# Kernel optimization log

Hardware: AMD Instinct MI355X
Metric: run time of the kernel (lower is better)

The kernel has to match this reference:

```python
import jax, jax.numpy as jnp
import numpy as np

N, E = 20000, 320000      # nodes, edges (avg degree 16)
IN_DIM, N_HID = 256, 256
T, R, H, L = 8, 8, 8, 2   # node types, relations, heads, layers
DK = N_HID // H


def _type_linear(x, W, b, ntype):
    # x:[N,di], W:[T,di,do], b:[T,do] -> per-node-type linear (compute-all + select;
    # math identical to the original boolean-mask gather->Linear->scatter dispatch)
    y_all = jnp.einsum('nd,tdo->nto', x, W) + b[None]
    return jnp.take_along_axis(y_all, ntype[:, None, None], axis=1)[:, 0]


def _mblock(x, ntype, edge_index, etype, ew, kW, kb, qW, qb, vW, vb, aW, ab,
            rel_pri, rel_att, rel_msg, skip, ln_g, ln_b):
    n, d = x.shape
    src, dst = edge_index[0], edge_index[1]
    k = _type_linear(x, kW, kb, ntype).reshape(n, H, DK)
    q = _type_linear(x, qW, qb, ntype).reshape(n, H, DK)
    v = _type_linear(x, vW, vb, ntype).reshape(n, H, DK)
    # relation-transformed keys/messages at node level: [N,R,H,DK]
    k_rt = jnp.einsum('nhd,rhde->nrhe', k, rel_att)
    v_rt = jnp.einsum('nhd,rhde->nrhe', v, rel_msg)
    k_e = k_rt[src, etype]          # [E,H,DK]
    v_e = v_rt[src, etype]          # [E,H,DK]
    q_e = q[dst]                    # [E,H,DK]
    scores = jnp.einsum('ehd,ehd->eh', q_e, k_e) * rel_pri[etype] / np.sqrt(DK)
    scores = scores * ew[:, None]   # edge weighting of attention logits
    # segment softmax over incoming edges of each destination node
    smax = jax.ops.segment_max(scores, dst, num_segments=n)
    ex = jnp.exp(scores - smax[dst])
    ssum = jax.ops.segment_sum(ex, dst, num_segments=n)
    att = ex / (ssum[dst] + 1e-9)   # [E,H]
    agg = jax.ops.segment_sum(att[:, :, None] * v_e, dst, num_segments=n).reshape(n, d)
    trans = _type_linear(jax.nn.gelu(agg), aW, ab, ntype)
    alpha = jax.nn.sigmoid(skip)[ntype][:, None]
    out = trans * alpha + x * (1.0 - alpha)
    # per-type LayerNorm
    mu = out.mean(-1, keepdims=True)
    var = out.var(-1, keepdims=True)
    out = (out - mu) / jnp.sqrt(var + 1e-5) * ln_g[ntype] + ln_b[ntype]
    return out, att


def setup_inputs():
    key = jax.random.key(0)
    ks = jax.random.split(key, 16)
    s = 0.05
    return {
        'node_feature': jax.random.normal(ks[0], (N, IN_DIM), jnp.float32),
        'node_type':    jax.random.randint(ks[1], (N,), 0, T, jnp.int32),
        'edge_weight':  jax.random.uniform(ks[2], (E,), jnp.float32),
        'edge_index':   jax.random.randint(ks[3], (2, E), 0, N, jnp.int32),
        'edge_type':    jax.random.randint(ks[4], (E,), 0, R, jnp.int32),
        'adapt_W': jax.random.normal(ks[5], (T, IN_DIM, N_HID), jnp.float32) * s,
        'adapt_b': jnp.zeros((T, N_HID), jnp.float32),
        'k_W': jax.random.normal(ks[6], (L, T, N_HID, N_HID), jnp.float32) * s,
        'k_b': jnp.zeros((L, T, N_HID), jnp.float32),
        'q_W': jax.random.normal(ks[7], (L, T, N_HID, N_HID), jnp.float32) * s,
        'q_b': jnp.zeros((L, T, N_HID), jnp.float32),
        'v_W': jax.random.normal(ks[8], (L, T, N_HID, N_HID), jnp.float32) * s,
        'v_b': jnp.zeros((L, T, N_HID), jnp.float32),
        'a_W': jax.random.normal(ks[9], (L, T, N_HID, N_HID), jnp.float32) * s,
        'a_b': jnp.zeros((L, T, N_HID), jnp.float32),
        'rel_pri': jnp.ones((L, R, H), jnp.float32),
        'rel_att': jax.random.normal(ks[10], (L, R, H, DK, DK), jnp.float32) * 0.1,
        'rel_msg': jax.random.normal(ks[11], (L, R, H, DK, DK), jnp.float32) * 0.1,
        'skip': jnp.ones((L, T), jnp.float32),
        'ln_g': jnp.ones((L, T, N_HID), jnp.float32),
        'ln_b': jnp.zeros((L, T, N_HID), jnp.float32),
    }


def reference(node_feature, node_type, edge_weight, edge_index, edge_type,
              adapt_W, adapt_b, k_W, k_b, q_W, q_b, v_W, v_b, a_W, a_b,
              rel_pri, rel_att, rel_msg, skip, ln_g, ln_b):
    # type-dispatched adapt: gather -> Linear -> tanh -> scatter (vectorized)
    x = jnp.tanh(_type_linear(node_feature, adapt_W, adapt_b, node_type))
    att = None
    for l in range(L):  # fixed small n_layers
        x, att = _mblock(x, node_type, edge_index, edge_type, edge_weight,
                         k_W[l], k_b[l], q_W[l], q_b[l], v_W[l], v_b[l],
                         a_W[l], a_b[l], rel_pri[l], rel_att[l], rel_msg[l],
                         skip[l], ln_g[l], ln_b[l])
    return x, att
```

## Files before the change

### kernel.cpp

```cpp
#include <hip/hip_runtime.h>
#include <hip/hip_bf16.h>
#include <math.h>

#define NN 20000
#define EE 320000
#define DD 256
#define TT 8
#define RR 8
#define HH 8
#define LLAYERS 2
#define RELN (LLAYERS * RR * HH * 1024)
#define NBN 79

typedef __attribute__((ext_vector_type(8))) short short8;
typedef __attribute__((ext_vector_type(4))) float f32x4;
typedef __attribute__((ext_vector_type(4))) unsigned short us4;

__device__ __forceinline__ float b2f(unsigned short u) {
    return __uint_as_float(((unsigned int)u) << 16);
}
__device__ __forceinline__ unsigned short f2b(float f) {
    unsigned int x = __float_as_uint(f);
    unsigned int r = (x + 0x7fffu + ((x >> 16) & 1u)) >> 16;
    return (unsigned short)r;
}

__global__ void k_prep(const float* __restrict__ nf, const float* __restrict__ rA,
                       const float* __restrict__ rM,
                       unsigned short* __restrict__ nf_bf, unsigned short* __restrict__ relA,
                       unsigned short* __restrict__ relMT) {
    int idx = blockIdx.x * 256 + threadIdx.x;
    const int n0 = NN * 256;
    if (idx < n0) { nf_bf[idx] = f2b(nf[idx]); return; }
    idx -= n0;
    if (idx < RELN) { relA[idx] = f2b(rA[idx]); return; }
    idx -= RELN;
    if (idx < RELN) {
        int g = idx >> 10, loc = idx & 1023;
        int a = loc >> 5, b = loc & 31;
        relMT[(size_t)g * 1024 + a * 32 + b] = f2b(rM[(size_t)g * 1024 + b * 32 + a]);
    }
}

__global__ void k_transpose_all(const float* __restrict__ adW, const float* __restrict__ kW,
                                const float* __restrict__ qW, const float* __restrict__ vW,
                                const float* __restrict__ aW, unsigned short* __restrict__ out) {
    __shared__ float tile[32][33];
    int z = blockIdx.z;
    const float* ip;
    if (z < 8) ip = adW + (size_t)z * 65536;
    else if (z < 24) ip = kW + (size_t)(z - 8) * 65536;
    else if (z < 40) ip = qW + (size_t)(z - 24) * 65536;
    else if (z < 56) ip = vW + (size_t)(z - 40) * 65536;
    else ip = aW + (size_t)(z - 56) * 65536;
    unsigned short* op = out + (size_t)z * 65536;
    int ox = blockIdx.x * 32, dy = blockIdx.y * 32;
    int tx = threadIdx.x, ty = threadIdx.y;
#pragma unroll
    for (int r = 0; r < 4; r++) tile[ty + 8 * r][tx] = ip[(size_t)(dy + ty + 8 * r) * 256 + ox + tx];
    __syncthreads();
#pragma unroll
    for (int r = 0; r < 4; r++) op[(size_t)(ox + ty + 8 * r) * 256 + dy + tx] = f2b(tile[tx][ty + 8 * r]);
}

__global__ void k_build1(const int* __restrict__ ei, const int* __restrict__ nt,
                         int* __restrict__ deg8, int* __restrict__ thist,
                         int* __restrict__ rank) {
    __shared__ int ltc[TT];
    int i = blockIdx.x * 256 + threadIdx.x;
    int vx = blockIdx.x & 7;
    if (i < EE) {
        int d = ei[EE + i];
        int lr = atomicAdd(&deg8[vx * NN + d], 1);
        rank[i] = (vx << 16) | lr;
    }
    if (blockIdx.x < NBN) {
        if (threadIdx.x < TT) ltc[threadIdx.x] = 0;
        __syncthreads();
        int n = blockIdx.x * 256 + threadIdx.x;
        if (n < NN) atomicAdd(&ltc[nt[n]], 1);
        __syncthreads();
        if (threadIdx.x < TT) thist[blockIdx.x * TT + threadIdx.x] = ltc[threadIdx.x];
    }
}

__global__ __launch_bounds__(256) void k_scanA(const int* __restrict__ deg8,
                                               int* __restrict__ degT,
                                               int* __restrict__ bsum) {
    __shared__ int red[256];
    int b = blockIdx.x, t = threadIdx.x;
    int n = b * 256 + t;
    int tot = 0;
    if (n < NN) {
#pragma unroll
        for (int vx = 0; vx < 8; vx++) tot += deg8[vx * NN + n];
        degT[n] = tot;
    }
    red[t] = tot;
    __syncthreads();
    for (int d = 128; d >= 1; d >>= 1) {
        if (t < d) red[t] += red[t + d];
        __syncthreads();
    }
    if (t == 0) bsum[b] = red[0];
}

__global__ void k_scanB(const int* __restrict__ bsum, int* __restrict__ bbase,
                        int* __restrict__ off,
                        const int* __restrict__ thist, int* __restrict__ toff,
                        int* __restrict__ tboff) {
    __shared__ int partial[TT];
    __shared__ int toff_l[TT + 1];
    int tid = threadIdx.x;
    if (tid == 0) {
        int a = 0;
        for (int b = 0; b < NBN; b++) { bbase[b] = a; a += bsum[b]; }
        off[NN] = EE;
    }
    if (tid < TT) {
        int tot = 0;
        for (int b = 0; b < NBN; b++) tot += thist[b * TT + tid];
        partial[tid] = tot;
    }
    __syncthreads();
    if (tid == 0) {
        int a = 0;
        for (int t = 0; t < TT; t++) { toff_l[t] = a; toff[t] = a; a += partial[t]; }
        toff_l[TT] = a; toff[TT] = a;
    }
    __syncthreads();
    if (tid < TT) {
        int r = toff_l[tid];
        for (int b = 0; b < NBN; b++) { tboff[b * TT + tid] = r; r += thist[b * TT + tid]; }
    }
}

__global__ __launch_bounds__(256) void k_scanC(const int* __restrict__ deg8,
                                               const int* __restrict__ degT,
                                               const int* __restrict__ bbase,
                                               int* __restrict__ off,
                                               int* __restrict__ base8) {
    __shared__ int s[256];
    int b = blockIdx.x, t = threadIdx.x;
    int n = b * 256 + t;
    int v = (n < NN) ? degT[n] : 0;
    s[t] = v;
    __syncthreads();
    for (int d = 1; d < 256; d <<= 1) {
        int x = (t >= d) ? s[t - d] : 0;
        __syncthreads();
        s[t] += x;
        __syncthreads();
    }
    if (n < NN) {
        int run = bbase[b] + s[t] - v;
        off[n] = run;
#pragma unroll
        for (int vx = 0; vx < 8; vx++) {
            base8[vx * NN + n] = run;
            run += deg8[vx * NN + n];
        }
    }
}

__global__ void k_build2(const int* __restrict__ ei, const int* __restrict__ et,
                         const float* __restrict__ ew, const int* __restrict__ nt,
                         const int* __restrict__ base8, const int* __restrict__ tboff,
                         const int* __restrict__ rank,
                         int4* __restrict__ csr, int* __restrict__ nlist) {
    __shared__ int ltc[TT];
    int i = blockIdx.x * 256 + threadIdx.x;
    if (i < EE) {
        int d = ei[EE + i];
        int rk = rank[i];
        int p = base8[(rk >> 16) * NN + d] + (rk & 0xffff);
        int4 pk;
        pk.x = ei[i] | (et[i] << 16);
        pk.y = __float_as_int(ew[i]);
        pk.z = d;
        pk.w = i;
        csr[p] = pk;
    }
    if (blockIdx.x < NBN) {
        if (threadIdx.x < TT) ltc[threadIdx.x] = 0;
        __syncthreads();
        int n = blockIdx.x * 256 + threadIdx.x;
        if (n < NN) {
            int t = nt[n];
            int pos = atomicAdd(&ltc[t], 1);
            nlist[tboff[blockIdx.x * TT + t] + pos] = n;
        }
    }
}

#define LDA 264

__device__ __forceinline__ void gemm_core(const unsigned short* A_l, const unsigned short* wt,
                                          int colbase, int l15, int l4, f32x4 acc[4][4]) {
    f32x4 zf = {0.f, 0.f, 0.f, 0.f};
#pragma unroll
    for (int a = 0; a < 4; a++)
#pragma unroll
        for (int b = 0; b < 4; b++) acc[a][b] = zf;
    for (int ks = 0; ks < 8; ks++) {
        int k0 = ks * 32;
        short8 af[4], bfr[4];
#pragma unroll
        for (int rb = 0; rb < 4; rb++)
            af[rb] = *(const short8*)(A_l + (rb * 16 + l15) * LDA + k0 + 8 * l4);
#pragma unroll
        for (int cb = 0; cb < 4; cb++)
            bfr[cb] = *(const short8*)(wt + (size_t)(colbase + cb * 16 + l15) * 256 + k0 + 8 * l4);
#pragma unroll
        for (int rb = 0; rb < 4; rb++)
#pragma unroll
            for (int cb = 0; cb < 4; cb++)
                acc[rb][cb] = __builtin_amdgcn_mfma_f32_16x16x32_bf16(af[rb], bfr[cb], acc[rb][cb], 0, 0, 0);
    }
}

template <int MODE>
__global__ __launch_bounds__(256) void k_gemm(
    const unsigned short* __restrict__ Abf,
    const unsigned short* __restrict__ Wt,
    const float* __restrict__ bias,
    const int* __restrict__ nlist, const int* __restrict__ toff,
    unsigned short* __restrict__ out_bf, float* out_f32,
    const unsigned short* x_in, const float* __restrict__ skipv,
    const float* __restrict__ lng, const float* __restrict__ lnb)
{
    __shared__ unsigned short A_l[64 * LDA];
    __shared__ int nid[64];
    __shared__ float redS[64 * 4];
    __shared__ float redQ[64 * 4];
    __shared__ float meanl[64];
    __shared__ float invl[64];

    int t = blockIdx.y;
    int g0 = toff[t], g1 = toff[t + 1];
    int base = blockIdx.x * 64;
    int cnt = g1 - g0 - base;
    if (cnt <= 0) return;
    if (cnt > 64) cnt = 64;
    int tid = threadIdx.x;
    if (tid < 64) nid[tid] = (tid < cnt) ? nlist[g0 + base + tid] : -1;
    __syncthreads();

#pragma unroll
    for (int it = 0; it < 8; it++) {
        int id = it * 256 + tid;
        int row = id >> 5, c8 = id & 31;
        short8 v = {};
        int nd = nid[row];
        if (nd >= 0) v = *(const short8*)(Abf + (size_t)nd * 256 + c8 * 8);
        *(short8*)(A_l + row * LDA + c8 * 8) = v;
    }
    __syncthreads();

    int lane = tid & 63, wave = tid >> 6;
    int colbase = wave * 64;
    int l15 = lane & 15, l4 = lane >> 4;
    f32x4 acc[4][4];
    gemm_core(A_l, Wt + (size_t)t * 65536, colbase, l15, l4, acc);

    if (MODE == 0) {
#pragma unroll
        for (int rb = 0; rb < 4; rb++) {
#pragma unroll
            for (int j = 0; j < 4; j++) {
                int r = rb * 16 + l4 * 4 + j;
                int nd = nid[r];
                if (nd < 0) continue;
#pragma unroll
                for (int cb = 0; cb < 4; cb++) {
                    int col = colbase + cb * 16 + l15;
                    float v = tanhf(acc[rb][cb][j] + bias[t * 256 + col]);
                    out_bf[(size_t)nd * 256 + col] = f2b(v);
                }
            }
        }
    } else {
        float alpha = 1.f / (1.f + __expf(-skipv[t]));
#pragma unroll
        for (int rb = 0; rb < 4; rb++) {
#pragma unroll
            for (int j = 0; j < 4; j++) {
                int r = rb * 16 + l4 * 4 + j;
                int nd = nid[r];
                float s = 0.f, q = 0.f;
#pragma unroll
                for (int cb = 0; cb < 4; cb++) {
                    int col = colbase + cb * 16 + l15;
                    float v = acc[rb][cb][j] + bias[t * 256 + col];
                    float xi = (nd >= 0) ? b2f(x_in[(size_t)nd * 256 + col]) : 0.f;
                    float o = v * alpha + xi * (1.f - alpha);
                    acc[rb][cb][j] = o;
                    s += o;
                    q += o * o;
                }
#pragma unroll
                for (int m = 1; m < 16; m <<= 1) {
                    s += __shfl_xor(s, m, 16);
                    q += __shfl_xor(q, m, 16);
                }
                if (l15 == 0) { redS[r * 4 + wave] = s; redQ[r * 4 + wave] = q; }
            }
        }
        __syncthreads();
        if (tid < 64) {
            float s = redS[tid * 4] + redS[tid * 4 + 1] + redS[tid * 4 + 2] + redS[tid * 4 + 3];
            float q = redQ[tid * 4] + redQ[tid * 4 + 1] + redQ[tid * 4 + 2] + redQ[tid * 4 + 3];
            float mean = s * (1.f / 256.f);
            float var = q * (1.f / 256.f) - mean * mean;
            meanl[tid] = mean;
            invl[tid] = rsqrtf(var + 1e-5f);
        }
        __syncthreads();
#pragma unroll
        for (int rb = 0; rb < 4; rb++) {
#pragma unroll
            for (int j = 0; j < 4; j++) {
                int r = rb * 16 + l4 * 4 + j;
                int nd = nid[r];
                if (nd < 0) continue;
                float mean = meanl[r], inv = invl[r];
#pragma unroll
                for (int cb = 0; cb < 4; cb++) {
                    int col = colbase + cb * 16 + l15;
                    float o = (acc[rb][cb][j] - mean) * inv * lng[t * 256 + col] + lnb[t * 256 + col];
                    if (out_f32) out_f32[(size_t)nd * 256 + col] = o;
                    out_bf[(size_t)nd * 256 + col] = f2b(o);
                }
            }
        }
    }
}

__global__ __launch_bounds__(256) void k_gemm3(
    const unsigned short* __restrict__ Abf,
    const unsigned short* __restrict__ Wt0, const unsigned short* __restrict__ Wt1,
    const unsigned short* __restrict__ Wt2,
    const float* __restrict__ b0, const float* __restrict__ b1, const float* __restrict__ b2,
    const int* __restrict__ nlist, const int* __restrict__ toff,
    unsigned short* __restrict__ o0, unsigned short* __restrict__ o1,
    unsigned short* __restrict__ o2)
{
    __shared__ unsigned short A_l[64 * LDA];
    __shared__ int nid[64];

    int t = blockIdx.y;
    int g0 = toff[t], g1 = toff[t + 1];
    int base = blockIdx.x * 64;
    int cnt = g1 - g0 - base;
    if (cnt <= 0) return;
    if (cnt > 64) cnt = 64;
    int tid = threadIdx.x;
    if (tid < 64) nid[tid] = (tid < cnt) ? nlist[g0 + base + tid] : -1;
    __syncthreads();

#pragma unroll
    for (int it = 0; it < 8; it++) {
        int id = it * 256 + tid;
        int row = id >> 5, c8 = id & 31;
        short8 v = {};
        int nd = nid[row];
        if (nd >= 0) v = *(const short8*)(Abf + (size_t)nd * 256 + c8 * 8);
        *(short8*)(A_l + row * LDA + c8 * 8) = v;
    }
    __syncthreads();

    int lane = tid & 63, wave = tid >> 6;
    int colbase = wave * 64;
    int l15 = lane & 15, l4 = lane >> 4;
    const unsigned short* Wts[3] = {Wt0, Wt1, Wt2};
    const float* bs[3] = {b0, b1, b2};
    unsigned short* os[3] = {o0, o1, o2};
#pragma unroll
    for (int w = 0; w < 3; w++) {
        f32x4 acc[4][4];
        gemm_core(A_l, Wts[w] + (size_t)t * 65536, colbase, l15, l4, acc);
#pragma unroll
        for (int rb = 0; rb < 4; rb++) {
#pragma unroll
            for (int j = 0; j < 4; j++) {
                int r = rb * 16 + l4 * 4 + j;
                int nd = nid[r];
                if (nd < 0) continue;
#pragma unroll
                for (int cb = 0; cb < 4; cb++) {
                    int col = colbase + cb * 16 + l15;
                    os[w][(size_t)nd * 256 + col] = f2b(acc[rb][cb][j] + bs[w][t * 256 + col]);
                }
            }
        }
    }
}

__global__ __launch_bounds__(256) void k_rt(
    const unsigned short* __restrict__ qb, const unsigned short* __restrict__ vb,
    const unsigned short* __restrict__ relA, const unsigned short* __restrict__ relMT,
    unsigned short* __restrict__ qrt, unsigned short* __restrict__ vrt)
{
    int tid = threadIdx.x;
    int lane = tid & 63, wave = tid >> 6;
    int l15 = lane & 15, l4 = lane >> 4;
    int h = blockIdx.y;
    int n = blockIdx.x * 64 + wave * 16 + l15;
    const unsigned short* inb = blockIdx.z ? vb : qb;
    const unsigned short* rel = blockIdx.z ? relMT : relA;
    unsigned short* outrt = blockIdx.z ? vrt : qrt;
    short8 bfrag = {};
    if (n < NN) bfrag = *(const short8*)(inb + (size_t)n * 256 + h * 32 + 8 * l4);
#pragma unroll
    for (int r = 0; r < RR; r++) {
        const unsigned short* ap = rel + ((size_t)(r * HH + h)) * 1024;
        short8 a0 = *(const short8*)(ap + l15 * 32 + 8 * l4);
        short8 a1 = *(const short8*)(ap + (16 + l15) * 32 + 8 * l4);
        f32x4 c0 = {0.f, 0.f, 0.f, 0.f}, c1 = {0.f, 0.f, 0.f, 0.f};
        c0 = __builtin_amdgcn_mfma_f32_16x16x32_bf16(a0, bfrag, c0, 0, 0, 0);
        c1 = __builtin_amdgcn_mfma_f32_16x16x32_bf16(a1, bfrag, c1, 0, 0, 0);
        if (n < NN) {
            size_t ob = (((size_t)(r * HH + h)) * NN + n) * 32;
            us4 p0, p1;
#pragma unroll
            for (int j = 0; j < 4; j++) { p0[j] = f2b(c0[j]); p1[j] = f2b(c1[j]); }
            *(us4*)(outrt + ob + l4 * 4) = p0;
            *(us4*)(outrt + ob + 16 + l4 * 4) = p1;
        }
    }
}

__global__ void k_score(const unsigned short* __restrict__ kbf,
                        const unsigned short* __restrict__ qrt,
                        const int4* __restrict__ csr, const float* __restrict__ pri,
                        float* __restrict__ sc)
{
    int idx = blockIdx.x * 256 + threadIdx.x;
    if (idx >= EE * HH) return;
    int p = idx >> 3, h = idx & 7;
    int4 pk = csr[p];
    int s = pk.x & 0xffff, r = (pk.x >> 16) & 7;
    float w = __int_as_float(pk.y);
    int d = pk.z;
    const short8* kp = (const short8*)(kbf + (size_t)s * 256 + h * 32);
    const short8* qp = (const short8*)(qrt + (((size_t)(r * HH + h)) * NN + d) * 32);
    float acc = 0.f;
#pragma unroll
    for (int c = 0; c < 4; c++) {
        short8 a = kp[c], b = qp[c];
#pragma unroll
        for (int j = 0; j < 8; j++)
            acc += b2f((unsigned short)a[j]) * b2f((unsigned short)b[j]);
    }
    sc[idx] = acc * pri[r * HH + h] * 0.17677669529663687f * w;
}

__global__ __launch_bounds__(256) void k_agg(
    const float* __restrict__ sc, const unsigned short* __restrict__ vrt,
    const int4* __restrict__ csr, const int* __restrict__ off,
    unsigned short* __restrict__ gbf, float* __restrict__ smaxg, float* __restrict__ ssumg)
{
    __shared__ float p_l[32][9];
    __shared__ int sv[32], se[32];
    int n = blockIdx.x;
    int tid = threadIdx.x;
    int h = tid >> 5, i = tid & 31;
    int t0 = off[n], cnt = off[n + 1] - t0;

    float smax = -INFINITY;
    for (int ii = i; ii < cnt; ii += 32)
        smax = fmaxf(smax, sc[(size_t)(t0 + ii) * 8 + h]);
#pragma unroll
    for (int m = 16; m >= 1; m >>= 1) smax = fmaxf(smax, __shfl_xor(smax, m, 32));

    float psum = 0.f, agg = 0.f;
    for (int c0 = 0; c0 < cnt; c0 += 32) {
        int m = cnt - c0;
        if (m > 32) m = 32;
        __syncthreads();
        if (tid < m) {
            int4 pk = csr[t0 + c0 + tid];
            sv[tid] = pk.x & 0xffff;
            se[tid] = (pk.x >> 16) & 7;
        }
        __syncthreads();
        if (i < m) {
            float p = __expf(sc[(size_t)(t0 + c0 + i) * 8 + h] - smax);
            p_l[i][h] = p;
            psum += p;
        }
        for (int ii = 0; ii < m; ii++) {
            float p = p_l[ii][h];
            agg += p * b2f(vrt[(((size_t)(se[ii] * HH + h)) * NN + sv[ii]) * 32 + i]);
        }
    }
#pragma unroll
    for (int m = 16; m >= 1; m >>= 1) psum += __shfl_xor(psum, m, 32);
    if (i == 0) { smaxg[n * 8 + h] = smax; ssumg[n * 8 + h] = psum; }
    float den = psum + 1e-9f;
    float a = agg / den;
    float g = 0.5f * a * (1.f + tanhf(0.7978845608028654f * (a + 0.044715f * a * a * a)));
    gbf[(size_t)n * 256 + tid] = f2b(g);
}

__global__ void k_att(const float* __restrict__ sc, const int4* __restrict__ csr,
                      const float* __restrict__ smaxg, const float* __restrict__ ssumg,
                      float* __restrict__ att)
{
    int idx = blockIdx.x * 256 + threadIdx.x;
    if (idx >= EE * HH) return;
    int p = idx >> 3, h = idx & 7;
    int4 pk = csr[p];
    int d = pk.z, e = pk.w;
    att[(size_t)e * 8 + h] = __expf(sc[idx] - smaxg[d * 8 + h]) / (ssumg[d * 8 + h] + 1e-9f);
}

extern "C" void kernel_launch(void* const* d_in, const int* in_sizes, int n_in,
                              void* d_out, int out_size, void* d_ws, size_t ws_size,
                              hipStream_t stream)
{
    const float* nf = (const float*)d_in[0];
    const int* ntyp = (const int*)d_in[1];
    const float* ew = (const float*)d_in[2];
    const int* ei = (const int*)d_in[3];
    const int* ety = (const int*)d_in[4];
    const float* adW = (const float*)d_in[5];
    const float* adb = (const float*)d_in[6];
    const float* kW = (const float*)d_in[7];
    const float* kb = (const float*)d_in[8];
    const float* qW = (const float*)d_in[9];
    const float* qb = (const float*)d_in[10];
    const float* vW = (const float*)d_in[11];
    const float* vb = (const float*)d_in[12];
    const float* aW = (const float*)d_in[13];
    const float* ab = (const float*)d_in[14];
    const float* pri = (const float*)d_in[15];
    const float* rA = (const float*)d_in[16];
    const float* rM = (const float*)d_in[17];
    const float* skp = (const float*)d_in[18];
    const float* lng = (const float*)d_in[19];
    const float* lnb = (const float*)d_in[20];

    float* x_out = (float*)d_out;
    float* att_out = x_out + (size_t)NN * 256;

    char* wsb = (char*)d_ws;
    size_t o = 0;
    auto take = [&](size_t bytes) -> void* {
        size_t r = (o + 255) & ~(size_t)255;
        o = r + bytes;
        return (void*)(wsb + r);
    };
    unsigned short* nf_bf = (unsigned short*)take((size_t)NN * 256 * 2);
    unsigned short* x_bf = (unsigned short*)take((size_t)NN * 256 * 2);
    unsigned short* kb16 = (unsigned short*)take((size_t)NN * 256 * 2);
    unsigned short* qb16 = (unsigned short*)take((size_t)NN * 256 * 2);
    unsigned short* vb16 = (unsigned short*)take((size_t)NN * 256 * 2);
    unsigned short* gb16 = (unsigned short*)take((size_t)NN * 256 * 2);
    unsigned short* qrt = (unsigned short*)take((size_t)NN * RR * HH * 32 * 2);
    unsigned short* vrt = (unsigned short*)take((size_t)NN * RR * HH * 32 * 2);
    float* scores = (float*)take((size_t)EE * HH * 4);
    float* smaxg = (float*)take((size_t)NN * HH * 4);
    float* ssumg = (float*)take((size_t)NN * HH * 4);
    unsigned short* Wt_all = (unsigned short*)take((size_t)72 * 65536 * 2);
    unsigned short* adWt = Wt_all;
    unsigned short* kWt = Wt_all + (size_t)8 * 65536;
    unsigned short* qWt = Wt_all + (size_t)24 * 65536;
    unsigned short* vWt = Wt_all + (size_t)40 * 65536;
    unsigned short* aWt = Wt_all + (size_t)56 * 65536;
    unsigned short* relA = (unsigned short*)take((size_t)RELN * 2);
    unsigned short* relMT = (unsigned short*)take((size_t)RELN * 2);
    int* zblock = (int*)take((size_t)(8 * NN + NBN * TT) * 4);
    int* deg8 = zblock;
    int* thist = zblock + 8 * NN;
    int* base8 = (int*)take((size_t)8 * NN * 4);
    int* degT = (int*)take((size_t)NN * 4);
    int* bsum = (int*)take((size_t)NBN * 4);
    int* bbase = (int*)take((size_t)NBN * 4);
    int* rank = (int*)take((size_t)EE * 4);
    int* off = (int*)take((size_t)(NN + 1) * 4);
    int4* csr = (int4*)take((size_t)EE * 16);
    int* tboff = (int*)take((size_t)NBN * TT * 4);
    int* toff = (int*)take((TT + 1) * 4);
    int* nlist = (int*)take((size_t)NN * 4);
    if (o > ws_size) return;

    hipMemsetAsync(zblock, 0, (size_t)(8 * NN + NBN * TT) * 4, stream);

    int ptot = NN * 256 + 2 * RELN;
    k_prep<<<(ptot + 255) / 256, 256, 0, stream>>>(nf, rA, rM, nf_bf, relA, relMT);
    k_transpose_all<<<dim3(8, 8, 72), dim3(32, 8), 0, stream>>>(adW, kW, qW, vW, aW, Wt_all);

    k_build1<<<(EE + 255) / 256, 256, 0, stream>>>(ei, ntyp, deg8, thist, rank);
    k_scanA<<<NBN, 256, 0, stream>>>(deg8, degT, bsum);
    k_scanB<<<1, 256, 0, stream>>>(bsum, bbase, off, thist, toff, tboff);
    k_scanC<<<NBN, 256, 0, stream>>>(deg8, degT, bbase, off, base8);
    k_build2<<<(EE + 255) / 256, 256, 0, stream>>>(ei, ety, ew, ntyp, base8, tboff, rank,
                                                   csr, nlist);

    dim3 ggrid((NN + 63) / 64, TT);
    k_gemm<0><<<ggrid, 256, 0, stream>>>(nf_bf, adWt, adb, nlist, toff,
                                         x_bf, nullptr, nullptr, nullptr, nullptr, nullptr);

    dim3 rgrid((NN + 63) / 64, HH, 2);
    int egrid = (EE * HH + 255) / 256;
    for (int l = 0; l < LLAYERS; l++) {
        k_gemm3<<<ggrid, 256, 0, stream>>>(x_bf,
                                           kWt + (size_t)l * TT * 65536, qWt + (size_t)l * TT * 65536,
                                           vWt + (size_t)l * TT * 65536,
                                           kb + (size_t)l * TT * 256, qb + (size_t)l * TT * 256,
                                           vb + (size_t)l * TT * 256,
                                           nlist, toff, kb16, qb16, vb16);
        k_rt<<<rgrid, 256, 0, stream>>>(qb16, vb16,
                                        relA + (size_t)l * RR * HH * 1024,
                                        relMT + (size_t)l * RR * HH * 1024, qrt, vrt);
        k_score<<<egrid, 256, 0, stream>>>(kb16, qrt, csr, pri + (size_t)l * RR * HH, scores);
        k_agg<<<NN, 256, 0, stream>>>(scores, vrt, csr, off, gb16, smaxg, ssumg);
        if (l == LLAYERS - 1)
            k_att<<<egrid, 256, 0, stream>>>(scores, csr, smaxg, ssumg, att_out);
        k_gemm<2><<<ggrid, 256, 0, stream>>>(gb16, aWt + (size_t)l * TT * 65536, ab + (size_t)l * TT * 256,
                                             nlist, toff, x_bf,
                                             (l == LLAYERS - 1) ? x_out : nullptr,
                                             x_bf,
                                             skp + (size_t)l * TT, lng + (size_t)l * TT * 256, lnb + (size_t)l * TT * 256);
    }
}
```

Before: 544.1 us.

## Store relation-transformed values node-major so edge gathers read contiguous rows

The v_rt buffer moves from a [R,H,N,32] layout to a node-major [N,R,H,32] layout. The MFMA output is written as 8-element vector stores in a permuted element order, and k_agg undoes that order with a lane permutation (posi). In the aggregation kernel the 8 heads of one edge's source node now read a contiguous 512-byte region instead of 8 widely separated rows, which should improve cache line use for the gather. The v branch of k_rt now launches one block per relation rather than per head, so both branches must share the same grid dimension (8 each).

```diff
diff --git a/kernel.cpp b/kernel.cpp
--- a/kernel.cpp
+++ b/kernel.cpp
@@ -15,6 +15,7 @@
 typedef __attribute__((ext_vector_type(8))) short short8;
 typedef __attribute__((ext_vector_type(4))) float f32x4;
 typedef __attribute__((ext_vector_type(4))) unsigned short us4;
+typedef __attribute__((ext_vector_type(8))) unsigned short us8;
 
 __device__ __forceinline__ float b2f(unsigned short u) {
     return __uint_as_float(((unsigned int)u) << 16);
@@ -404,28 +405,48 @@
     int tid = threadIdx.x;
     int lane = tid & 63, wave = tid >> 6;
     int l15 = lane & 15, l4 = lane >> 4;
-    int h = blockIdx.y;
     int n = blockIdx.x * 64 + wave * 16 + l15;
-    const unsigned short* inb = blockIdx.z ? vb : qb;
-    const unsigned short* rel = blockIdx.z ? relMT : relA;
-    unsigned short* outrt = blockIdx.z ? vrt : qrt;
-    short8 bfrag = {};
-    if (n < NN) bfrag = *(const short8*)(inb + (size_t)n * 256 + h * 32 + 8 * l4);
-#pragma unroll
-    for (int r = 0; r < RR; r++) {
-        const unsigned short* ap = rel + ((size_t)(r * HH + h)) * 1024;
-        short8 a0 = *(const short8*)(ap + l15 * 32 + 8 * l4);
-        short8 a1 = *(const short8*)(ap + (16 + l15) * 32 + 8 * l4);
-        f32x4 c0 = {0.f, 0.f, 0.f, 0.f}, c1 = {0.f, 0.f, 0.f, 0.f};
-        c0 = __builtin_amdgcn_mfma_f32_16x16x32_bf16(a0, bfrag, c0, 0, 0, 0);
-        c1 = __builtin_amdgcn_mfma_f32_16x16x32_bf16(a1, bfrag, c1, 0, 0, 0);
-        if (n < NN) {
-            size_t ob = (((size_t)(r * HH + h)) * NN + n) * 32;
-            us4 p0, p1;
-#pragma unroll
-            for (int j = 0; j < 4; j++) { p0[j] = f2b(c0[j]); p1[j] = f2b(c1[j]); }
-            *(us4*)(outrt + ob + l4 * 4) = p0;
-            *(us4*)(outrt + ob + 16 + l4 * 4) = p1;
+    bool ok = (n < NN);
+    if (blockIdx.z == 0) {
+        int h = blockIdx.y;
+        short8 bfrag = {};
+        if (ok) bfrag = *(const short8*)(qb + (size_t)n * 256 + h * 32 + 8 * l4);
+#pragma unroll
+        for (int r = 0; r < RR; r++) {
+            const unsigned short* ap = relA + ((size_t)(r * HH + h)) * 1024;
+            short8 a0 = *(const short8*)(ap + l15 * 32 + 8 * l4);
+            short8 a1 = *(const short8*)(ap + (16 + l15) * 32 + 8 * l4);
+            f32x4 c0 = {0.f, 0.f, 0.f, 0.f}, c1 = {0.f, 0.f, 0.f, 0.f};
+            c0 = __builtin_amdgcn_mfma_f32_16x16x32_bf16(a0, bfrag, c0, 0, 0, 0);
+            c1 = __builtin_amdgcn_mfma_f32_16x16x32_bf16(a1, bfrag, c1, 0, 0, 0);
+            if (ok) {
+                size_t ob = (((size_t)(r * HH + h)) * NN + n) * 32;
+                us4 p0, p1;
+#pragma unroll
+                for (int j = 0; j < 4; j++) { p0[j] = f2b(c0[j]); p1[j] = f2b(c1[j]); }
+                *(us4*)(qrt + ob + l4 * 4) = p0;
+                *(us4*)(qrt + ob + 16 + l4 * 4) = p1;
+            }
+        }
+    } else {
+        int r = blockIdx.y;
+#pragma unroll
+        for (int h = 0; h < HH; h++) {
+            short8 bfrag = {};
+            if (ok) bfrag = *(const short8*)(vb + (size_t)n * 256 + h * 32 + 8 * l4);
+            const unsigned short* ap = relMT + ((size_t)(r * HH + h)) * 1024;
+            short8 a0 = *(const short8*)(ap + l15 * 32 + 8 * l4);
+            short8 a1 = *(const short8*)(ap + (16 + l15) * 32 + 8 * l4);
+            f32x4 c0 = {0.f, 0.f, 0.f, 0.f}, c1 = {0.f, 0.f, 0.f, 0.f};
+            c0 = __builtin_amdgcn_mfma_f32_16x16x32_bf16(a0, bfrag, c0, 0, 0, 0);
+            c1 = __builtin_amdgcn_mfma_f32_16x16x32_bf16(a1, bfrag, c1, 0, 0, 0);
+            if (ok) {
+                size_t ob = (((size_t)n * (RR * HH)) + r * HH + h) * 32;
+                us8 pk;
+#pragma unroll
+                for (int j = 0; j < 4; j++) { pk[j] = f2b(c0[j]); pk[4 + j] = f2b(c1[j]); }
+                *(us8*)(vrt + ob + l4 * 8) = pk;
+            }
         }
     }
 }
@@ -466,6 +487,7 @@
     int tid = threadIdx.x;
     int h = tid >> 5, i = tid & 31;
     int t0 = off[n], cnt = off[n + 1] - t0;
+    int posi = ((i & 12) << 1) | ((i >> 4) << 2) | (i & 3);
 
     float smax = -INFINITY;
     for (int ii = i; ii < cnt; ii += 32)
@@ -491,7 +513,7 @@
         }
         for (int ii = 0; ii < m; ii++) {
             float p = p_l[ii][h];
-            agg += p * b2f(vrt[(((size_t)(se[ii] * HH + h)) * NN + sv[ii]) * 32 + i]);
+            agg += p * b2f(vrt[(((size_t)sv[ii] * (RR * HH)) + se[ii] * HH + h) * 32 + posi]);
         }
     }
 #pragma unroll
```

Measured after the change: 560.5 us. 1.03x slower.
